# Optimization experiments

Measured on AMD Instinct MI355X. Metric: run time of the kernel, lower is better.

Reference implementation:

```python
import jax, jax.numpy as jnp
import numpy as np

N_NODES = 50000
N_EDGES = 800000
D_IN = 64
D_HID = 64
D_OUT = 64


def setup_inputs() -> dict:
    key = jax.random.key(0)
    ks = jax.random.split(key, 9)
    x = jax.random.normal(ks[0], (N_NODES, D_IN), dtype=jnp.float32)
    src = jax.random.randint(ks[1], (N_EDGES,), 0, N_NODES, dtype=jnp.int64)
    dst = jax.random.randint(ks[2], (N_EDGES,), 0, N_NODES, dtype=jnp.int64)
    s0 = 1.0 / np.sqrt(D_IN)
    s1 = 1.0 / np.sqrt(D_HID)
    W_self0 = jax.random.normal(ks[3], (D_IN, D_HID), dtype=jnp.float32) * s0
    W_neigh0 = jax.random.normal(ks[4], (D_IN, D_HID), dtype=jnp.float32) * s0
    b0 = jnp.zeros((D_HID,), dtype=jnp.float32)
    W_self1 = jax.random.normal(ks[5], (D_HID, D_OUT), dtype=jnp.float32) * s1
    W_neigh1 = jax.random.normal(ks[6], (D_HID, D_OUT), dtype=jnp.float32) * s1
    b1 = jnp.zeros((D_OUT,), dtype=jnp.float32)
    return {"x": x, "src": src, "dst": dst,
            "W_self0": W_self0, "W_neigh0": W_neigh0, "b0": b0,
            "W_self1": W_self1, "W_neigh1": W_neigh1, "b1": b1}


def reference(x, src, dst, W_self0, W_neigh0, b0, W_self1, W_neigh1, b1):
    n = x.shape[0]
    # in-degree per destination node; clamp to 1 for isolated nodes (DGL behavior)
    deg = jax.ops.segment_sum(jnp.ones(src.shape[0], dtype=x.dtype), dst, num_segments=n)
    inv_deg = (1.0 / jnp.maximum(deg, 1.0))[:, None]  # [N,1]

    def sage_mean(h, W_self, W_neigh, b):
        # gather src features, mean-reduce onto dst, then linear combine
        agg = jax.ops.segment_sum(h[src], dst, num_segments=n)  # [N,d]
        neigh = agg * inv_deg
        return h @ W_self + neigh @ W_neigh + b

    # layer 0: SAGEConv with internal relu activation
    h = jax.nn.relu(sage_mean(x, W_self0, W_neigh0, b0))
    # outer relu in GraphSAGE_Full.forward (idempotent after internal relu)
    h = jax.nn.relu(h)
    # dropout rate 0.0 -> identity
    # final layer: no activation
    h = sage_mean(h, W_self1, W_neigh1, b1)
    return h
```

## Files before the change

### kernel.cpp

```cpp
#include <hip/hip_runtime.h>

#define N_NODES 50000
#define N_EDGES 800000
#define D 64
#define NSLICE 8
#define SLICE_N ((N_NODES + NSLICE - 1) / NSLICE)
#define BCAP 64

__device__ __forceinline__ unsigned short f2bf(float f) {
    unsigned int u = __builtin_bit_cast(unsigned int, f);
    u += 0x7fffu + ((u >> 16) & 1u);
    return (unsigned short)(u >> 16);
}
__device__ __forceinline__ float bflo(unsigned int u) {
    return __builtin_bit_cast(float, u << 16);
}
__device__ __forceinline__ float bfhi(unsigned int u) {
    return __builtin_bit_cast(float, u & 0xffff0000u);
}

__device__ __forceinline__ void xform_body(const float* __restrict__ h,
        const float* __restrict__ Ws, const float* __restrict__ Wn,
        const float* __restrict__ b,
        float* __restrict__ yS, unsigned short* __restrict__ yN,
        int gwave, int nwaves, int lane) {
    int mat = gwave & 1;
    const float* W = mat ? Wn : Ws;

    float w[D];
#pragma unroll
    for (int k = 0; k < D; ++k) w[k] = W[k * D + lane];
    float bj = mat ? 0.f : b[lane];

    const int ngroups = (N_NODES + 3) / 4;
    for (int g = gwave >> 1; g < ngroups; g += (nwaves >> 1)) {
        const float* x0 = h + (size_t)(g * 4) * D;
        float a0 = bj, a1 = bj, a2 = bj, a3 = bj;
#pragma unroll
        for (int kq = 0; kq < 16; ++kq) {
            float4 v0 = *(const float4*)(x0 + 0 * D + kq * 4);
            float4 v1 = *(const float4*)(x0 + 1 * D + kq * 4);
            float4 v2 = *(const float4*)(x0 + 2 * D + kq * 4);
            float4 v3 = *(const float4*)(x0 + 3 * D + kq * 4);
            a0 = fmaf(v0.x, w[kq * 4 + 0], a0);
            a1 = fmaf(v1.x, w[kq * 4 + 0], a1);
            a2 = fmaf(v2.x, w[kq * 4 + 0], a2);
            a3 = fmaf(v3.x, w[kq * 4 + 0], a3);
            a0 = fmaf(v0.y, w[kq * 4 + 1], a0);
            a1 = fmaf(v1.y, w[kq * 4 + 1], a1);
            a2 = fmaf(v2.y, w[kq * 4 + 1], a2);
            a3 = fmaf(v3.y, w[kq * 4 + 1], a3);
            a0 = fmaf(v0.z, w[kq * 4 + 2], a0);
            a1 = fmaf(v1.z, w[kq * 4 + 2], a1);
            a2 = fmaf(v2.z, w[kq * 4 + 2], a2);
            a3 = fmaf(v3.z, w[kq * 4 + 2], a3);
            a0 = fmaf(v0.w, w[kq * 4 + 3], a0);
            a1 = fmaf(v1.w, w[kq * 4 + 3], a1);
            a2 = fmaf(v2.w, w[kq * 4 + 3], a2);
            a3 = fmaf(v3.w, w[kq * 4 + 3], a3);
        }
        size_t base = (size_t)(g * 4) * D + lane;
        if (mat) {
            yN[base + 0 * D] = f2bf(a0);
            yN[base + 1 * D] = f2bf(a1);
            yN[base + 2 * D] = f2bf(a2);
            yN[base + 3 * D] = f2bf(a3);
        } else {
            yS[base + 0 * D] = a0;
            yS[base + 1 * D] = a1;
            yS[base + 2 * D] = a2;
            yS[base + 3 * D] = a3;
        }
    }
}

__global__ __launch_bounds__(256) void k_pre(const float* __restrict__ x,
        const float* __restrict__ Ws0, const float* __restrict__ Wn0,
        const float* __restrict__ b0,
        float* __restrict__ yS, unsigned short* __restrict__ yN,
        const int* __restrict__ src, const int* __restrict__ dst,
        int* __restrict__ cnt, int* __restrict__ csr) {
    int bid = (int)blockIdx.x;
    if (bid < 1024) {
        int lane = threadIdx.x & 63;
        int gwave = __builtin_amdgcn_readfirstlane(bid * 4 + (int)(threadIdx.x >> 6));
        xform_body(x, Ws0, Wn0, b0, yS, yN, gwave, 4096, lane);
    } else {
        int slice = bid & 7;
        int lo = slice * SLICE_N, hi = lo + SLICE_N;
        int gblk = (bid - 1024) >> 3;
        const int4* d4p = (const int4*)dst;
        const int4* s4p = (const int4*)src;
        const int NV = N_EDGES / 4;
        for (int v = gblk * 256 + (int)threadIdx.x; v < NV; v += 128 * 256) {
            int4 d4 = d4p[v];
            int4 s4 = s4p[v];
            if (d4.x >= lo && d4.x < hi) { int p = atomicAdd(&cnt[d4.x], 1); csr[(d4.x << 6) + p] = s4.x; }
            if (d4.y >= lo && d4.y < hi) { int p = atomicAdd(&cnt[d4.y], 1); csr[(d4.y << 6) + p] = s4.y; }
            if (d4.z >= lo && d4.z < hi) { int p = atomicAdd(&cnt[d4.z], 1); csr[(d4.z << 6) + p] = s4.z; }
            if (d4.w >= lo && d4.w < hi) { int p = atomicAdd(&cnt[d4.w], 1); csr[(d4.w << 6) + p] = s4.w; }
        }
    }
}

__global__ __launch_bounds__(256, 4) void k_xform(const float* __restrict__ h,
        const float* __restrict__ Ws, const float* __restrict__ Wn,
        const float* __restrict__ b,
        float* __restrict__ yS, unsigned short* __restrict__ yN) {
    int lane = threadIdx.x & 63;
    int gwave = __builtin_amdgcn_readfirstlane((blockIdx.x * blockDim.x + threadIdx.x) >> 6);
    int nwaves = (gridDim.x * blockDim.x) >> 6;
    xform_body(h, Ws, Wn, b, yS, yN, gwave, nwaves, lane);
}

__global__ __launch_bounds__(256) void k_aggf(const char* __restrict__ yN,
        const float* __restrict__ yS,
        const int* __restrict__ cnt, const int* __restrict__ csr,
        float* __restrict__ out, int relu) {
    int node = __builtin_amdgcn_readfirstlane((blockIdx.x * blockDim.x + threadIdx.x) >> 6);
    int lane = threadIdx.x & 63;
    int q = lane >> 3;
    int fq = lane & 7;
    int deg = cnt[node];
    const int* bucket = csr + (node << 6);
    unsigned foff = (unsigned)fq * 16u;

    float s0 = 0.f, s1 = 0.f, s2 = 0.f, s3 = 0.f;
    float s4 = 0.f, s5 = 0.f, s6 = 0.f, s7 = 0.f;

#define ROUND16(E0)                                                         \
    {                                                                       \
        int i0 = (E0) + q, i1 = i0 + 8;                                     \
        int b0 = bucket[i0], b1 = bucket[i1];                               \
        unsigned a0 = (i0 < deg) ? ((unsigned)b0 << 7) : 0u;                \
        unsigned a1 = (i1 < deg) ? ((unsigned)b1 << 7) : 0u;                \
        float m0 = (i0 < deg) ? 1.f : 0.f;                                  \
        float m1 = (i1 < deg) ? 1.f : 0.f;                                  \
        uint4 u0 = *(const uint4*)(yN + a0 + foff);                         \
        uint4 u1 = *(const uint4*)(yN + a1 + foff);                         \
        s0 = fmaf(m0, bflo(u0.x), s0); s0 = fmaf(m1, bflo(u1.x), s0);       \
        s1 = fmaf(m0, bfhi(u0.x), s1); s1 = fmaf(m1, bfhi(u1.x), s1);       \
        s2 = fmaf(m0, bflo(u0.y), s2); s2 = fmaf(m1, bflo(u1.y), s2);       \
        s3 = fmaf(m0, bfhi(u0.y), s3); s3 = fmaf(m1, bfhi(u1.y), s3);       \
        s4 = fmaf(m0, bflo(u0.z), s4); s4 = fmaf(m1, bflo(u1.z), s4);       \
        s5 = fmaf(m0, bfhi(u0.z), s5); s5 = fmaf(m1, bfhi(u1.z), s5);       \
        s6 = fmaf(m0, bflo(u0.w), s6); s6 = fmaf(m1, bflo(u1.w), s6);       \
        s7 = fmaf(m0, bfhi(u0.w), s7); s7 = fmaf(m1, bfhi(u1.w), s7);       \
    }

    ROUND16(0)
    if (deg > 16) ROUND16(16)
    if (deg > 32) {
        ROUND16(32)
        if (deg > 48) ROUND16(48)
    }
#undef ROUND16

    s0 += __shfl_xor(s0, 8, 64); s0 += __shfl_xor(s0, 16, 64); s0 += __shfl_xor(s0, 32, 64);
    s1 += __shfl_xor(s1, 8, 64); s1 += __shfl_xor(s1, 16, 64); s1 += __shfl_xor(s1, 32, 64);
    s2 += __shfl_xor(s2, 8, 64); s2 += __shfl_xor(s2, 16, 64); s2 += __shfl_xor(s2, 32, 64);
    s3 += __shfl_xor(s3, 8, 64); s3 += __shfl_xor(s3, 16, 64); s3 += __shfl_xor(s3, 32, 64);
    s4 += __shfl_xor(s4, 8, 64); s4 += __shfl_xor(s4, 16, 64); s4 += __shfl_xor(s4, 32, 64);
    s5 += __shfl_xor(s5, 8, 64); s5 += __shfl_xor(s5, 16, 64); s5 += __shfl_xor(s5, 32, 64);
    s6 += __shfl_xor(s6, 8, 64); s6 += __shfl_xor(s6, 16, 64); s6 += __shfl_xor(s6, 32, 64);
    s7 += __shfl_xor(s7, 8, 64); s7 += __shfl_xor(s7, 16, 64); s7 += __shfl_xor(s7, 32, 64);

    float sv = (q == 0) ? s0 : (q == 1) ? s1 : (q == 2) ? s2 : (q == 3) ? s3
             : (q == 4) ? s4 : (q == 5) ? s5 : (q == 6) ? s6 : s7;
    int f = fq * 8 + q;
    float self = yS[(size_t)node * D + f];
    float inv = 1.0f / fmaxf((float)deg, 1.0f);
    float acc = self + sv * inv;
    if (relu) acc = fmaxf(acc, 0.f);
    out[(size_t)node * D + f] = acc;
}

extern "C" void kernel_launch(void* const* d_in, const int* in_sizes, int n_in,
                              void* d_out, int out_size, void* d_ws, size_t ws_size,
                              hipStream_t stream) {
    const float* x   = (const float*)d_in[0];
    const int*   src = (const int*)d_in[1];
    const int*   dst = (const int*)d_in[2];
    const float* Ws0 = (const float*)d_in[3];
    const float* Wn0 = (const float*)d_in[4];
    const float* b0  = (const float*)d_in[5];
    const float* Ws1 = (const float*)d_in[6];
    const float* Wn1 = (const float*)d_in[7];
    const float* b1  = (const float*)d_in[8];
    float* out = (float*)d_out;

    char* p = (char*)d_ws;
    float*          yS  = (float*)p;          p += (size_t)N_NODES * D * sizeof(float);
    unsigned short* yN  = (unsigned short*)p; p += (size_t)N_NODES * D * sizeof(unsigned short);
    int* cnt = (int*)p;                       p += (size_t)N_NODES * sizeof(int);
    int* csr = (int*)p;                       p += (size_t)N_NODES * BCAP * sizeof(int);

    const int aggBlocks = (N_NODES + 3) / 4;

    hipMemsetAsync(cnt, 0, (size_t)N_NODES * sizeof(int), stream);

    k_pre<<<2048, 256, 0, stream>>>(x, Ws0, Wn0, b0, yS, yN, src, dst, cnt, csr);

    k_aggf<<<aggBlocks, 256, 0, stream>>>((const char*)yN, yS, cnt, csr, out, 1);

    k_xform<<<1024, 256, 0, stream>>>(out, Ws1, Wn1, b1, yS, yN);
    k_aggf<<<aggBlocks, 256, 0, stream>>>((const char*)yN, yS, cnt, csr, out, 0);
}
```

Before: 185.7 us.

## Rewrite layer-1 transform as row-per-lane tiles with wave-uniform weight loads

The second-layer dense transform now assigns one node row to each lane, with each wave handling a 64-row tile, one weight matrix (self or neighbour) and half of the output columns. Weight rows are read as wave-uniform 16-float vectors and accumulated in registers, replacing the earlier shared xform_body grid-stride scheme. The goal is to raise parallelism (one block per tile) and turn weight reads into scalar/broadcast loads. In exchange, each lane keeps a full 64-float input row plus accumulators in registers, which raises register pressure, and stores are per-lane strided rows, which may be less coalesced.

```diff
diff --git a/kernel.cpp b/kernel.cpp
--- a/kernel.cpp
+++ b/kernel.cpp
@@ -6,6 +6,9 @@
 #define NSLICE 8
 #define SLICE_N ((N_NODES + NSLICE - 1) / NSLICE)
 #define BCAP 64
+#define NTILE ((N_NODES + 63) / 64)
+
+typedef float floatx16 __attribute__((ext_vector_type(16)));
 
 __device__ __forceinline__ unsigned short f2bf(float f) {
     unsigned int u = __builtin_bit_cast(unsigned int, f);
@@ -103,14 +106,67 @@
     }
 }
 
-__global__ __launch_bounds__(256, 4) void k_xform(const float* __restrict__ h,
+__global__ __launch_bounds__(256) void k_xform(const float* __restrict__ h,
         const float* __restrict__ Ws, const float* __restrict__ Wn,
         const float* __restrict__ b,
         float* __restrict__ yS, unsigned short* __restrict__ yN) {
     int lane = threadIdx.x & 63;
-    int gwave = __builtin_amdgcn_readfirstlane((blockIdx.x * blockDim.x + threadIdx.x) >> 6);
-    int nwaves = (gridDim.x * blockDim.x) >> 6;
-    xform_body(h, Ws, Wn, b, yS, yN, gwave, nwaves, lane);
+    int gwave = __builtin_amdgcn_readfirstlane((int)((blockIdx.x * blockDim.x + threadIdx.x) >> 6));
+    int mat  = gwave & 1;
+    int jh   = (gwave >> 1) & 1;
+    int tile = gwave >> 2;
+    if (tile >= NTILE) return;
+    const float* W = mat ? Wn : Ws;
+
+    int row = tile * 64 + lane;
+    int lrow = row < N_NODES ? row : N_NODES - 1;
+    bool live = row < N_NODES;
+    const float* hr = h + (size_t)lrow * D;
+
+    float4 hv[16];
+#pragma unroll
+    for (int kq = 0; kq < 16; ++kq) hv[kq] = *(const float4*)(hr + kq * 4);
+
+    for (int jb = 0; jb < 2; ++jb) {
+        int j0 = jh * 32 + jb * 16;
+        float acc[16];
+#pragma unroll
+        for (int j = 0; j < 16; ++j) acc[j] = mat ? 0.f : b[j0 + j];
+
+#pragma unroll
+        for (int kq = 0; kq < 16; ++kq) {
+#pragma unroll
+            for (int c = 0; c < 4; ++c) {
+                float hk = (c == 0) ? hv[kq].x : (c == 1) ? hv[kq].y
+                         : (c == 2) ? hv[kq].z : hv[kq].w;
+                floatx16 wv = *(const floatx16*)(W + (kq * 4 + c) * D + j0);
+#pragma unroll
+                for (int j = 0; j < 16; ++j) acc[j] = fmaf(hk, wv[j], acc[j]);
+            }
+        }
+
+        if (live) {
+            if (mat) {
+                unsigned p0 = (unsigned)f2bf(acc[0])  | ((unsigned)f2bf(acc[1])  << 16);
+                unsigned p1 = (unsigned)f2bf(acc[2])  | ((unsigned)f2bf(acc[3])  << 16);
+                unsigned p2 = (unsigned)f2bf(acc[4])  | ((unsigned)f2bf(acc[5])  << 16);
+                unsigned p3 = (unsigned)f2bf(acc[6])  | ((unsigned)f2bf(acc[7])  << 16);
+                unsigned p4 = (unsigned)f2bf(acc[8])  | ((unsigned)f2bf(acc[9])  << 16);
+                unsigned p5 = (unsigned)f2bf(acc[10]) | ((unsigned)f2bf(acc[11]) << 16);
+                unsigned p6 = (unsigned)f2bf(acc[12]) | ((unsigned)f2bf(acc[13]) << 16);
+                unsigned p7 = (unsigned)f2bf(acc[14]) | ((unsigned)f2bf(acc[15]) << 16);
+                uint4* dst0 = (uint4*)(yN + (size_t)row * D + j0);
+                dst0[0] = make_uint4(p0, p1, p2, p3);
+                dst0[1] = make_uint4(p4, p5, p6, p7);
+            } else {
+                float4* dst0 = (float4*)(yS + (size_t)row * D + j0);
+                dst0[0] = make_float4(acc[0],  acc[1],  acc[2],  acc[3]);
+                dst0[1] = make_float4(acc[4],  acc[5],  acc[6],  acc[7]);
+                dst0[2] = make_float4(acc[8],  acc[9],  acc[10], acc[11]);
+                dst0[3] = make_float4(acc[12], acc[13], acc[14], acc[15]);
+            }
+        }
+    }
 }
 
 __global__ __launch_bounds__(256) void k_aggf(const char* __restrict__ yN,
@@ -203,6 +259,6 @@
 
     k_aggf<<<aggBlocks, 256, 0, stream>>>((const char*)yN, yS, cnt, csr, out, 1);
 
-    k_xform<<<1024, 256, 0, stream>>>(out, Ws1, Wn1, b1, yS, yN);
+    k_xform<<<NTILE, 256, 0, stream>>>(out, Ws1, Wn1, b1, yS, yN);
     k_aggf<<<aggBlocks, 256, 0, stream>>>((const char*)yN, yS, cnt, csr, out, 0);
 }
```

New measurement: 188.8 us. Within noise of the previous version (+1.7%).

## Fuse layer-0 aggregation with layer-1 transform into a single kernel

Applied to the files above, without the earlier changes.

Replaces the layer-0 aggregation kernel and the separate layer-1 transform kernel with one kernel. Each wave processes 17 nodes, holds the layer-1 weights in registers, aggregates a node's neighbours, applies ReLU, and computes the self and neighbour projections through readlane broadcasts. This avoids writing and re-reading the intermediate hidden activations and saves a kernel launch. In exchange, it needs extra workspace buffers, uses many registers for the weights, and runs the per-node 64-step readlane loop serially, so occupancy and latency hiding may drop.

```diff
diff --git a/kernel.cpp b/kernel.cpp
--- a/kernel.cpp
+++ b/kernel.cpp
@@ -6,6 +6,9 @@
 #define NSLICE 8
 #define SLICE_N ((N_NODES + NSLICE - 1) / NSLICE)
 #define BCAP 64
+
+#define FAGG_BLOCKS 768
+#define NPW 17
 
 __device__ __forceinline__ unsigned short f2bf(float f) {
     unsigned int u = __builtin_bit_cast(unsigned int, f);
@@ -103,14 +106,92 @@
     }
 }
 
-__global__ __launch_bounds__(256, 4) void k_xform(const float* __restrict__ h,
-        const float* __restrict__ Ws, const float* __restrict__ Wn,
-        const float* __restrict__ b,
-        float* __restrict__ yS, unsigned short* __restrict__ yN) {
+#define ROUND16(E0)                                                         \
+    {                                                                       \
+        int i0 = (E0) + q, i1 = i0 + 8;                                     \
+        int b0_ = bucket[i0], b1_ = bucket[i1];                             \
+        unsigned a0 = (i0 < deg) ? ((unsigned)b0_ << 7) : 0u;               \
+        unsigned a1 = (i1 < deg) ? ((unsigned)b1_ << 7) : 0u;               \
+        float m0 = (i0 < deg) ? 1.f : 0.f;                                  \
+        float m1 = (i1 < deg) ? 1.f : 0.f;                                  \
+        uint4 u0 = *(const uint4*)(tb + a0 + foff);                         \
+        uint4 u1 = *(const uint4*)(tb + a1 + foff);                         \
+        s0 = fmaf(m0, bflo(u0.x), s0); s0 = fmaf(m1, bflo(u1.x), s0);       \
+        s1 = fmaf(m0, bfhi(u0.x), s1); s1 = fmaf(m1, bfhi(u1.x), s1);       \
+        s2 = fmaf(m0, bflo(u0.y), s2); s2 = fmaf(m1, bflo(u1.y), s2);       \
+        s3 = fmaf(m0, bfhi(u0.y), s3); s3 = fmaf(m1, bfhi(u1.y), s3);       \
+        s4 = fmaf(m0, bflo(u0.z), s4); s4 = fmaf(m1, bflo(u1.z), s4);       \
+        s5 = fmaf(m0, bfhi(u0.z), s5); s5 = fmaf(m1, bfhi(u1.z), s5);       \
+        s6 = fmaf(m0, bflo(u0.w), s6); s6 = fmaf(m1, bflo(u1.w), s6);       \
+        s7 = fmaf(m0, bfhi(u0.w), s7); s7 = fmaf(m1, bfhi(u1.w), s7);       \
+    }
+
+__global__ __launch_bounds__(256) void k_fagg0(const char* __restrict__ yN0,
+        const float* __restrict__ yS0,
+        const int* __restrict__ cnt, const int* __restrict__ csr,
+        const float* __restrict__ Ws1, const float* __restrict__ Wn1,
+        const float* __restrict__ b1,
+        float* __restrict__ yS1, unsigned short* __restrict__ yN1) {
     int lane = threadIdx.x & 63;
-    int gwave = __builtin_amdgcn_readfirstlane((blockIdx.x * blockDim.x + threadIdx.x) >> 6);
-    int nwaves = (gridDim.x * blockDim.x) >> 6;
-    xform_body(h, Ws, Wn, b, yS, yN, gwave, nwaves, lane);
+    int wid = __builtin_amdgcn_readfirstlane((int)((blockIdx.x * blockDim.x + threadIdx.x) >> 6));
+    int q = lane >> 3;
+    int fq = lane & 7;
+    unsigned foff = (unsigned)fq * 16u;
+    int f = fq * 8 + q;
+
+    float ws[D], wn[D];
+#pragma unroll
+    for (int k = 0; k < D; ++k) ws[k] = Ws1[k * D + lane];
+#pragma unroll
+    for (int k = 0; k < D; ++k) wn[k] = Wn1[k * D + lane];
+    float bj = b1[lane];
+
+    int n0 = wid * NPW;
+    int n1 = n0 + NPW; if (n1 > N_NODES) n1 = N_NODES;
+    for (int node = n0; node < n1; ++node) {
+        int deg = cnt[node];
+        const int* bucket = csr + (node << 6);
+        const char* tb = yN0;
+
+        float s0 = 0.f, s1 = 0.f, s2 = 0.f, s3 = 0.f;
+        float s4 = 0.f, s5 = 0.f, s6 = 0.f, s7 = 0.f;
+
+        ROUND16(0)
+        if (deg > 16) ROUND16(16)
+        if (deg > 32) {
+            ROUND16(32)
+            if (deg > 48) ROUND16(48)
+        }
+
+        s0 += __shfl_xor(s0, 8, 64); s0 += __shfl_xor(s0, 16, 64); s0 += __shfl_xor(s0, 32, 64);
+        s1 += __shfl_xor(s1, 8, 64); s1 += __shfl_xor(s1, 16, 64); s1 += __shfl_xor(s1, 32, 64);
+        s2 += __shfl_xor(s2, 8, 64); s2 += __shfl_xor(s2, 16, 64); s2 += __shfl_xor(s2, 32, 64);
+        s3 += __shfl_xor(s3, 8, 64); s3 += __shfl_xor(s3, 16, 64); s3 += __shfl_xor(s3, 32, 64);
+        s4 += __shfl_xor(s4, 8, 64); s4 += __shfl_xor(s4, 16, 64); s4 += __shfl_xor(s4, 32, 64);
+        s5 += __shfl_xor(s5, 8, 64); s5 += __shfl_xor(s5, 16, 64); s5 += __shfl_xor(s5, 32, 64);
+        s6 += __shfl_xor(s6, 8, 64); s6 += __shfl_xor(s6, 16, 64); s6 += __shfl_xor(s6, 32, 64);
+        s7 += __shfl_xor(s7, 8, 64); s7 += __shfl_xor(s7, 16, 64); s7 += __shfl_xor(s7, 32, 64);
+
+        float sv = (q == 0) ? s0 : (q == 1) ? s1 : (q == 2) ? s2 : (q == 3) ? s3
+                 : (q == 4) ? s4 : (q == 5) ? s5 : (q == 6) ? s6 : s7;
+        float self = yS0[(size_t)node * D + f];
+        float inv = 1.0f / fmaxf((float)deg, 1.0f);
+        float hrow = fmaxf(self + sv * inv, 0.f);
+
+        float acc_s = bj;
+        float acc_n = 0.f;
+        unsigned hbits = __builtin_bit_cast(unsigned, hrow);
+#pragma unroll
+        for (int k = 0; k < D; ++k) {
+            unsigned hb = __builtin_amdgcn_readlane(hbits, ((k & 7) << 3) | (k >> 3));
+            float hk = __builtin_bit_cast(float, hb);
+            acc_s = fmaf(hk, ws[k], acc_s);
+            acc_n = fmaf(hk, wn[k], acc_n);
+        }
+
+        yS1[(size_t)node * D + lane] = acc_s;
+        yN1[(size_t)node * D + lane] = f2bf(acc_n);
+    }
 }
 
 __global__ __launch_bounds__(256) void k_aggf(const char* __restrict__ yN,
@@ -123,30 +204,11 @@
     int fq = lane & 7;
     int deg = cnt[node];
     const int* bucket = csr + (node << 6);
+    const char* tb = yN;
     unsigned foff = (unsigned)fq * 16u;
 
     float s0 = 0.f, s1 = 0.f, s2 = 0.f, s3 = 0.f;
     float s4 = 0.f, s5 = 0.f, s6 = 0.f, s7 = 0.f;
-
-#define ROUND16(E0)                                                         \
-    {                                                                       \
-        int i0 = (E0) + q, i1 = i0 + 8;                                     \
-        int b0 = bucket[i0], b1 = bucket[i1];                               \
-        unsigned a0 = (i0 < deg) ? ((unsigned)b0 << 7) : 0u;                \
-        unsigned a1 = (i1 < deg) ? ((unsigned)b1 << 7) : 0u;                \
-        float m0 = (i0 < deg) ? 1.f : 0.f;                                  \
-        float m1 = (i1 < deg) ? 1.f : 0.f;                                  \
-        uint4 u0 = *(const uint4*)(yN + a0 + foff);                         \
-        uint4 u1 = *(const uint4*)(yN + a1 + foff);                         \
-        s0 = fmaf(m0, bflo(u0.x), s0); s0 = fmaf(m1, bflo(u1.x), s0);       \
-        s1 = fmaf(m0, bfhi(u0.x), s1); s1 = fmaf(m1, bfhi(u1.x), s1);       \
-        s2 = fmaf(m0, bflo(u0.y), s2); s2 = fmaf(m1, bflo(u1.y), s2);       \
-        s3 = fmaf(m0, bfhi(u0.y), s3); s3 = fmaf(m1, bfhi(u1.y), s3);       \
-        s4 = fmaf(m0, bflo(u0.z), s4); s4 = fmaf(m1, bflo(u1.z), s4);       \
-        s5 = fmaf(m0, bfhi(u0.z), s5); s5 = fmaf(m1, bfhi(u1.z), s5);       \
-        s6 = fmaf(m0, bflo(u0.w), s6); s6 = fmaf(m1, bflo(u1.w), s6);       \
-        s7 = fmaf(m0, bfhi(u0.w), s7); s7 = fmaf(m1, bfhi(u1.w), s7);       \
-    }
 
     ROUND16(0)
     if (deg > 16) ROUND16(16)
@@ -154,7 +216,6 @@
         ROUND16(32)
         if (deg > 48) ROUND16(48)
     }
-#undef ROUND16
 
     s0 += __shfl_xor(s0, 8, 64); s0 += __shfl_xor(s0, 16, 64); s0 += __shfl_xor(s0, 32, 64);
     s1 += __shfl_xor(s1, 8, 64); s1 += __shfl_xor(s1, 16, 64); s1 += __shfl_xor(s1, 32, 64);
@@ -190,8 +251,10 @@
     float* out = (float*)d_out;
 
     char* p = (char*)d_ws;
-    float*          yS  = (float*)p;          p += (size_t)N_NODES * D * sizeof(float);
-    unsigned short* yN  = (unsigned short*)p; p += (size_t)N_NODES * D * sizeof(unsigned short);
+    float*          yS0 = (float*)p;          p += (size_t)N_NODES * D * sizeof(float);
+    unsigned short* yN0 = (unsigned short*)p; p += (size_t)N_NODES * D * sizeof(unsigned short);
+    float*          yS1 = (float*)p;          p += (size_t)N_NODES * D * sizeof(float);
+    unsigned short* yN1 = (unsigned short*)p; p += (size_t)N_NODES * D * sizeof(unsigned short);
     int* cnt = (int*)p;                       p += (size_t)N_NODES * sizeof(int);
     int* csr = (int*)p;                       p += (size_t)N_NODES * BCAP * sizeof(int);
 
@@ -199,10 +262,10 @@
 
     hipMemsetAsync(cnt, 0, (size_t)N_NODES * sizeof(int), stream);
 
-    k_pre<<<2048, 256, 0, stream>>>(x, Ws0, Wn0, b0, yS, yN, src, dst, cnt, csr);
-
-    k_aggf<<<aggBlocks, 256, 0, stream>>>((const char*)yN, yS, cnt, csr, out, 1);
-
-    k_xform<<<1024, 256, 0, stream>>>(out, Ws1, Wn1, b1, yS, yN);
-    k_aggf<<<aggBlocks, 256, 0, stream>>>((const char*)yN, yS, cnt, csr, out, 0);
-}
+    k_pre<<<2048, 256, 0, stream>>>(x, Ws0, Wn0, b0, yS0, yN0, src, dst, cnt, csr);
+
+    k_fagg0<<<FAGG_BLOCKS, 256, 0, stream>>>((const char*)yN0, yS0, cnt, csr,
+                                             Ws1, Wn1, b1, yS1, yN1);
+
+    k_aggf<<<aggBlocks, 256, 0, stream>>>((const char*)yN1, yS1, cnt, csr, out, 0);
+}
```

Result: slower. 221.5 us (+19.3%).
